# Kernel tuning notes

Measured on AMD Instinct MI355X. Metric: run time of the kernel, lower is better.

## Reference

```python
import jax, jax.numpy as jnp
import numpy as np

D_MODEL = 1024
D_FF = 4096
N_EXPERTS = 8
TOP_K = 2

def setup_inputs() -> dict:
    key = jax.random.key(0)
    ks = jax.random.split(key, 8)
    s = 1.0 / np.sqrt(D_MODEL)
    sf = 1.0 / np.sqrt(D_FF)
    return {
        "x": jax.random.normal(ks[0], (4, 1024, D_MODEL), dtype=jnp.float32),
        "W1": jax.random.uniform(ks[1], (N_EXPERTS, D_MODEL, D_FF), jnp.float32, -s, s),
        "b1": jax.random.uniform(ks[2], (N_EXPERTS, D_FF), jnp.float32, -s, s),
        "W2": jax.random.uniform(ks[3], (N_EXPERTS, D_FF, D_MODEL), jnp.float32, -sf, sf),
        "b2": jax.random.uniform(ks[4], (N_EXPERTS, D_MODEL), jnp.float32, -sf, sf),
        "Wg": jax.random.uniform(ks[5], (D_MODEL, N_EXPERTS), jnp.float32, -s, s),
        "bg": jax.random.uniform(ks[6], (N_EXPERTS,), jnp.float32, -s, s),
    }

def reference(x, W1, b1, W2, b2, Wg, bg):
    # gate: [B,S,E]
    logits = jnp.einsum('bsd,de->bse', x, Wg) + bg
    probs = jax.nn.softmax(logits, axis=-1)
    # top-k mask + renormalize (k < n_experts)
    topk_vals, topk_idx = jax.lax.top_k(probs, TOP_K)
    mask = jax.nn.one_hot(topk_idx, N_EXPERTS, dtype=probs.dtype).sum(axis=-2)
    probs = probs * mask
    denom = probs.sum(axis=-1, keepdims=True)
    denom = denom + (denom == 0).astype(probs.dtype)
    probs = probs / denom
    # dense expert compute: all experts on all tokens. h: [B,E,S,d_ff]
    h = jnp.einsum('bsd,edf->besf', x, W1) + b1[None, :, None, :]
    h = jax.nn.gelu(h, approximate=False)
    y = jnp.einsum('besf,efd->besd', h, W2) + b2[None, :, None, :]
    # weighted combine over experts: [B,S,d]
    out = jnp.einsum('bse,besd->bsd', probs, y)
    return out
```

## Files before the change

### kernel.cpp

```cpp
#include <hip/hip_runtime.h>
#include <hip/hip_bf16.h>

#define NTOK   4096
#define DMODEL 1024
#define DFF    4096
#define NEXP   8
#define TOPK   2
#define BM 128
#define BN 128
#define BK 64
#define NSLOT   (NTOK*TOPK)
#define MAXSLOT (NSLOT + NEXP*BM)
#define MAXTILE (MAXSLOT/BM)

typedef __attribute__((ext_vector_type(8))) short bf16x8;
typedef __attribute__((ext_vector_type(4))) float f32x4;

__device__ __forceinline__ unsigned short f2bf(float f){
    union { float f; unsigned int u; } v; v.f = f;
    unsigned int r = (v.u + 0x7fffu + ((v.u >> 16) & 1u)) >> 16;
    return (unsigned short)r;
}
__device__ __forceinline__ float bf2f(unsigned short h){
    union { unsigned int u; float f; } v; v.u = ((unsigned int)h) << 16;
    return v.f;
}

__device__ __forceinline__ void gload16(const unsigned short* g, unsigned short* l){
    __builtin_amdgcn_global_load_lds(
        (const __attribute__((address_space(1))) void*)g,
        (__attribute__((address_space(3))) void*)l,
        16, 0, 0);
}

__global__ __launch_bounds__(256) void k_convert(const float* __restrict__ src,
                                                 unsigned short* __restrict__ dst, int n4)
{
    int i = blockIdx.x*256 + threadIdx.x;
    if(i >= n4) return;
    float4 v = ((const float4*)src)[i];
    ushort4 o;
    o.x = f2bf(v.x); o.y = f2bf(v.y); o.z = f2bf(v.z); o.w = f2bf(v.w);
    ((ushort4*)dst)[i] = o;
}

__global__ __launch_bounds__(256) void k_transpose_convert(const float* __restrict__ src,
                                                           unsigned short* __restrict__ dst,
                                                           int R, int C)
{
    __shared__ unsigned short tile[64][72];
    src += (size_t)blockIdx.z * R * C;
    dst += (size_t)blockIdx.z * R * C;
    int r0 = blockIdx.y * 64, c0 = blockIdx.x * 64;
    int t = threadIdx.x;
    int tr = t >> 4;
    int tc = (t & 15) * 4;
    #pragma unroll
    for(int i=0;i<4;i++){
        float4 v = *(const float4*)&src[(size_t)(r0 + tr + i*16)*C + c0 + tc];
        tile[tc+0][tr + i*16] = f2bf(v.x);
        tile[tc+1][tr + i*16] = f2bf(v.y);
        tile[tc+2][tr + i*16] = f2bf(v.z);
        tile[tc+3][tr + i*16] = f2bf(v.w);
    }
    __syncthreads();
    #pragma unroll
    for(int i=0;i<4;i++){
        ushort4 o;
        o.x = tile[tr + i*16][tc+0];
        o.y = tile[tr + i*16][tc+1];
        o.z = tile[tr + i*16][tc+2];
        o.w = tile[tr + i*16][tc+3];
        *(ushort4*)&dst[(size_t)(c0 + tr + i*16)*R + r0 + tc] = o;
    }
}

__global__ __launch_bounds__(256) void k_gate(const float* __restrict__ x,
                                              const float* __restrict__ Wg,
                                              const float* __restrict__ bg,
                                              int* __restrict__ token_e,
                                              float* __restrict__ token_w,
                                              int* __restrict__ cnt)
{
    int wid = threadIdx.x >> 6, lane = threadIdx.x & 63;
    int t = blockIdx.x * 4 + wid;
    const float* xr = x + (size_t)t * DMODEL;
    float pe[NEXP];
    #pragma unroll
    for(int e=0;e<NEXP;e++) pe[e] = 0.f;
    for(int i=0;i<DMODEL/64;i++){
        int d = i*64 + lane;
        float xv = xr[d];
        const float* wr = Wg + (size_t)d * NEXP;
        #pragma unroll
        for(int e=0;e<NEXP;e++) pe[e] += xv * wr[e];
    }
    #pragma unroll
    for(int off=32; off>0; off>>=1){
        #pragma unroll
        for(int e=0;e<NEXP;e++) pe[e] += __shfl_xor(pe[e], off);
    }
    if(lane == 0){
        float lg[NEXP], mx = -1e30f;
        #pragma unroll
        for(int e=0;e<NEXP;e++){ lg[e] = pe[e] + bg[e]; mx = fmaxf(mx, lg[e]); }
        float pr[NEXP];
        #pragma unroll
        for(int e=0;e<NEXP;e++) pr[e] = expf(lg[e] - mx);
        int e0 = 0; float p0 = pr[0];
        #pragma unroll
        for(int e=1;e<NEXP;e++) if(pr[e] > p0){ p0 = pr[e]; e0 = e; }
        int e1 = -1; float p1 = -1.f;
        #pragma unroll
        for(int e=0;e<NEXP;e++) if(e != e0 && pr[e] > p1){ p1 = pr[e]; e1 = e; }
        float dn = p0 + p1;
        token_e[2*t]   = e0; token_w[2*t]   = p0/dn;
        token_e[2*t+1] = e1; token_w[2*t+1] = p1/dn;
        atomicAdd(&cnt[e0], 1); atomicAdd(&cnt[e1], 1);
    }
}

__global__ void k_prefix(const int* __restrict__ cnt, int* __restrict__ base,
                         int* __restrict__ cursor, int* __restrict__ tile_e,
                         int* __restrict__ tile_row0, int* __restrict__ tile_valid)
{
    if(threadIdx.x != 0 || blockIdx.x != 0) return;
    int off = 0, nt = 0;
    for(int e=0;e<NEXP;e++){
        base[e] = off; cursor[e] = 0;
        int c = cnt[e];
        for(int r=0;r<c;r+=BM){
            tile_e[nt] = e; tile_row0[nt] = off + r;
            tile_valid[nt] = (c - r < BM) ? (c - r) : BM;
            nt++;
        }
        off += ((c + BM - 1)/BM)*BM;
    }
    for(int i=nt;i<MAXTILE;i++){ tile_e[i]=0; tile_row0[i]=0; tile_valid[i]=0; }
}

__global__ __launch_bounds__(256) void k_scatter(const int* __restrict__ token_e,
                                                 const float* __restrict__ token_w,
                                                 const int* __restrict__ base,
                                                 int* __restrict__ cursor,
                                                 int* __restrict__ slot_token,
                                                 float* __restrict__ slot_w,
                                                 int* __restrict__ slot_of)
{
    int i = blockIdx.x*256 + threadIdx.x;
    if(i >= NSLOT) return;
    int e = token_e[i];
    int s = base[e] + atomicAdd(&cursor[e], 1);
    slot_token[s] = i >> 1;
    slot_w[s] = token_w[i];
    slot_of[i] = s;
}

template<bool GATHER, bool GELU>
__global__ __launch_bounds__(256) void k_gemm(const unsigned short* __restrict__ A,
                                              const unsigned short* __restrict__ Bw,
                                              const float* __restrict__ bias,
                                              const int* __restrict__ tile_e,
                                              const int* __restrict__ tile_row0,
                                              const int* __restrict__ tile_valid,
                                              const int* __restrict__ slot_token,
                                              const float* __restrict__ slot_w,
                                              unsigned short* __restrict__ Out,
                                              int K, int N)
{
    int tid = blockIdx.x;
    int valid = tile_valid[tid];
    if(valid == 0) return;
    int e = tile_e[tid];
    int row0 = tile_row0[tid];
    int n0 = blockIdx.y * BN;
    const unsigned short* Be = Bw + (size_t)e * N * K;

    __shared__ unsigned short As[BM*BK];
    __shared__ unsigned short Bs[BN*BK];

    int t = threadIdx.x;
    int lane = t & 63;
    int wid = t >> 6;
    int wr = wid >> 1, wc = wid & 1;

    int srow = t >> 3;
    int csw  = (t & 7) ^ (srow & 7);
    const unsigned short* arow[4];
    const unsigned short* brow[4];
    #pragma unroll
    for(int i=0;i<4;i++){
        int r = i*32 + srow;
        size_t aoff;
        if(GATHER) aoff = (size_t)slot_token[row0 + r] * (size_t)K;
        else       aoff = (size_t)(row0 + r) * (size_t)K;
        arow[i] = A  + aoff + csw*8;
        brow[i] = Be + (size_t)(n0 + r)*K + csw*8;
    }
    unsigned short* alds = As + (size_t)t * 8;
    unsigned short* blds = Bs + (size_t)t * 8;

    f32x4 acc[4][4];
    #pragma unroll
    for(int m=0;m<4;m++)
        #pragma unroll
        for(int n=0;n<4;n++)
            acc[m][n] = (f32x4){0.f,0.f,0.f,0.f};

    int rl = lane & 15;
    int g  = lane >> 4;
    int rx = rl & 7;

    for(int k0=0;k0<K;k0+=BK){
        __syncthreads();
        #pragma unroll
        for(int i=0;i<4;i++){
            gload16(arow[i] + k0, alds + i*2048);
            gload16(brow[i] + k0, blds + i*2048);
        }
        __syncthreads();

        #pragma unroll
        for(int kb=0;kb<2;kb++){
            int sw = ((kb*4 + g) ^ rx) * 8;
            bf16x8 af[4], bfv[4];
            #pragma unroll
            for(int m=0;m<4;m++) af[m]  = *(const bf16x8*)&As[(wr*64 + m*16 + rl)*BK + sw];
            #pragma unroll
            for(int n=0;n<4;n++) bfv[n] = *(const bf16x8*)&Bs[(wc*64 + n*16 + rl)*BK + sw];
            #pragma unroll
            for(int m=0;m<4;m++)
                #pragma unroll
                for(int n=0;n<4;n++)
                    acc[m][n] = __builtin_amdgcn_mfma_f32_16x16x32_bf16(af[m], bfv[n], acc[m][n], 0, 0, 0);
        }
    }

    const float* be = bias + (size_t)e * N;
    #pragma unroll
    for(int m=0;m<4;m++){
        int rb = wr*64 + m*16 + ((lane>>4)<<2);
        #pragma unroll
        for(int j=0;j<4;j++){
            int r = rb + j;
            if(r >= valid) continue;
            size_t grow = (size_t)(row0 + r);
            float wsc = GELU ? 0.f : slot_w[grow];
            #pragma unroll
            for(int n=0;n<4;n++){
                int col = n0 + wc*64 + n*16 + (lane & 15);
                float v = acc[m][n][j] + be[col];
                if(GELU) v = 0.5f * v * (1.f + erff(v * 0.70710678118654752f));
                else     v *= wsc;
                Out[grow * (size_t)N + col] = f2bf(v);
            }
        }
    }
}

__global__ __launch_bounds__(256) void k_combine(const int* __restrict__ slot_of,
                                                 const unsigned short* __restrict__ Y,
                                                 float* __restrict__ out)
{
    int i = blockIdx.x*256 + threadIdx.x;
    int t  = i >> 8;
    int cg = i & 255;
    int s0 = slot_of[2*t], s1 = slot_of[2*t+1];
    uint2 a = *((const uint2*)(Y + (size_t)s0*DMODEL) + cg);
    uint2 b = *((const uint2*)(Y + (size_t)s1*DMODEL) + cg);
    float4 o;
    o.x = bf2f((unsigned short)(a.x & 0xffffu)) + bf2f((unsigned short)(b.x & 0xffffu));
    o.y = bf2f((unsigned short)(a.x >> 16))     + bf2f((unsigned short)(b.x >> 16));
    o.z = bf2f((unsigned short)(a.y & 0xffffu)) + bf2f((unsigned short)(b.y & 0xffffu));
    o.w = bf2f((unsigned short)(a.y >> 16))     + bf2f((unsigned short)(b.y >> 16));
    *((float4*)(out + (size_t)t*DMODEL) + cg) = o;
}

extern "C" void kernel_launch(void* const* d_in, const int* in_sizes, int n_in,
                              void* d_out, int out_size, void* d_ws, size_t ws_size,
                              hipStream_t stream)
{
    const float* x  = (const float*)d_in[0];
    const float* W1 = (const float*)d_in[1];
    const float* b1 = (const float*)d_in[2];
    const float* W2 = (const float*)d_in[3];
    const float* b2 = (const float*)d_in[4];
    const float* Wg = (const float*)d_in[5];
    const float* bg = (const float*)d_in[6];
    float* out = (float*)d_out;

    char* p = (char*)d_ws;
    auto alloc = [&](size_t bytes)->char*{
        char* r = p; p += (bytes + 255) & ~(size_t)255; return r;
    };
    unsigned short* W1t = (unsigned short*)alloc((size_t)NEXP*DFF*DMODEL*2);
    unsigned short* W2t = (unsigned short*)alloc((size_t)NEXP*DMODEL*DFF*2);
    unsigned short* Xb  = (unsigned short*)alloc((size_t)NTOK*DMODEL*2);
    unsigned short* H   = (unsigned short*)alloc((size_t)MAXSLOT*DFF*2);
    unsigned short* Y   = (unsigned short*)alloc((size_t)MAXSLOT*DMODEL*2);
    int*   slot_token = (int*)alloc(MAXSLOT*4);
    float* slot_w     = (float*)alloc(MAXSLOT*4);
    int*   slot_of    = (int*)alloc(NSLOT*4);
    int*   token_e    = (int*)alloc(NSLOT*4);
    float* token_w    = (float*)alloc(NSLOT*4);
    int*   cnt    = (int*)alloc(32);
    int*   base   = (int*)alloc(32);
    int*   cursor = (int*)alloc(32);
    int*   tile_e     = (int*)alloc(MAXTILE*4);
    int*   tile_row0  = (int*)alloc(MAXTILE*4);
    int*   tile_valid = (int*)alloc(MAXTILE*4);
    (void)ws_size; (void)in_sizes; (void)n_in; (void)out_size;

    hipMemsetAsync(cnt, 0, 32, stream);
    hipMemsetAsync(slot_token, 0, MAXSLOT*4, stream);
    k_convert<<<(NTOK*DMODEL/4 + 255)/256, 256, 0, stream>>>(x, Xb, NTOK*DMODEL/4);
    k_transpose_convert<<<dim3(DFF/64, DMODEL/64, NEXP), 256, 0, stream>>>(W1, W1t, DMODEL, DFF);
    k_transpose_convert<<<dim3(DMODEL/64, DFF/64, NEXP), 256, 0, stream>>>(W2, W2t, DFF, DMODEL);
    k_gate<<<NTOK/4, 256, 0, stream>>>(x, Wg, bg, token_e, token_w, cnt);
    k_prefix<<<1, 64, 0, stream>>>(cnt, base, cursor, tile_e, tile_row0, tile_valid);
    k_scatter<<<NSLOT/256, 256, 0, stream>>>(token_e, token_w, base, cursor,
                                             slot_token, slot_w, slot_of);
    k_gemm<true, true ><<<dim3(MAXTILE, DFF/BN),    256, 0, stream>>>(
        Xb, W1t, b1, tile_e, tile_row0, tile_valid, slot_token, slot_w, H, DMODEL, DFF);
    k_gemm<false,false><<<dim3(MAXTILE, DMODEL/BN), 256, 0, stream>>>(
        H,  W2t, b2, tile_e, tile_row0, tile_valid, slot_token, slot_w, Y, DFF, DMODEL);
    k_combine<<<NTOK*DMODEL/4/256, 256, 0, stream>>>(slot_of, Y, out);
}
```

Baseline: 496.1 us.

## Rewrite grouped GEMM as 256x256 tile, 8-wave double-buffered pipelined MFMA kernel

Grows the expert GEMM tile to 256x256 with 512 threads and eight waves. Global-to-LDS loads are double-buffered and interleaved with MFMA phases, using explicit waitcnt, barriers and setprio so loads overlap compute. The x bf16 conversion moves into the gate kernel, prefix and scatter merge into one single-block kernel, and Y reuses the W1t buffer. Larger tiles raise data reuse but pad each expert group to 256 rows, which wastes more work, and the single-block scatter serialises that step.

```diff
diff --git a/kernel.cpp b/kernel.cpp
--- a/kernel.cpp
+++ b/kernel.cpp
@@ -6,9 +6,8 @@
 #define DFF    4096
 #define NEXP   8
 #define TOPK   2
-#define BM 128
-#define BN 128
-#define BK 64
+#define BM 256
+#define BN 256
 #define NSLOT   (NTOK*TOPK)
 #define MAXSLOT (NSLOT + NEXP*BM)
 #define MAXTILE (MAXSLOT/BM)
@@ -33,15 +32,15 @@
         16, 0, 0);
 }
 
-__global__ __launch_bounds__(256) void k_convert(const float* __restrict__ src,
-                                                 unsigned short* __restrict__ dst, int n4)
-{
-    int i = blockIdx.x*256 + threadIdx.x;
-    if(i >= n4) return;
-    float4 v = ((const float4*)src)[i];
-    ushort4 o;
-    o.x = f2bf(v.x); o.y = f2bf(v.y); o.z = f2bf(v.z); o.w = f2bf(v.w);
-    ((ushort4*)dst)[i] = o;
+#define WAITLGKM() asm volatile("s_waitcnt lgkmcnt(0)" ::: "memory")
+#define WAITVM4()  asm volatile("s_waitcnt vmcnt(4)" ::: "memory")
+#define WAITVM0()  asm volatile("s_waitcnt vmcnt(0)" ::: "memory")
+#define MFMA16(a,b,c) __builtin_amdgcn_mfma_f32_16x16x32_bf16(a,b,c,0,0,0)
+
+__device__ __forceinline__ bf16x8 ldswz(const unsigned short* lds, int base, int r, int kcol){
+    int idx = base + r*64 + kcol;
+    idx ^= ((r>>2)&1) << 4;
+    return *(const bf16x8*)&lds[idx];
 }
 
 __global__ __launch_bounds__(256) void k_transpose_convert(const float* __restrict__ src,
@@ -78,11 +77,22 @@
 __global__ __launch_bounds__(256) void k_gate(const float* __restrict__ x,
                                               const float* __restrict__ Wg,
                                               const float* __restrict__ bg,
+                                              unsigned short* __restrict__ Xb,
                                               int* __restrict__ token_e,
                                               float* __restrict__ token_w,
                                               int* __restrict__ cnt)
 {
-    int wid = threadIdx.x >> 6, lane = threadIdx.x & 63;
+    int tid = threadIdx.x;
+    const float4* xs = (const float4*)x + (size_t)blockIdx.x * 1024;
+    ushort4* xd = (ushort4*)Xb + (size_t)blockIdx.x * 1024;
+    #pragma unroll
+    for(int rep=0;rep<4;rep++){
+        float4 v = xs[rep*256 + tid];
+        ushort4 o; o.x=f2bf(v.x); o.y=f2bf(v.y); o.z=f2bf(v.z); o.w=f2bf(v.w);
+        xd[rep*256 + tid] = o;
+    }
+
+    int wid = tid >> 6, lane = tid & 63;
     int t = blockIdx.x * 4 + wid;
     const float* xr = x + (size_t)t * DMODEL;
     float pe[NEXP];
@@ -120,136 +130,204 @@
     }
 }
 
-__global__ void k_prefix(const int* __restrict__ cnt, int* __restrict__ base,
-                         int* __restrict__ cursor, int* __restrict__ tile_e,
-                         int* __restrict__ tile_row0, int* __restrict__ tile_valid)
-{
-    if(threadIdx.x != 0 || blockIdx.x != 0) return;
-    int off = 0, nt = 0;
-    for(int e=0;e<NEXP;e++){
-        base[e] = off; cursor[e] = 0;
-        int c = cnt[e];
-        for(int r=0;r<c;r+=BM){
-            tile_e[nt] = e; tile_row0[nt] = off + r;
-            tile_valid[nt] = (c - r < BM) ? (c - r) : BM;
-            nt++;
-        }
-        off += ((c + BM - 1)/BM)*BM;
-    }
-    for(int i=nt;i<MAXTILE;i++){ tile_e[i]=0; tile_row0[i]=0; tile_valid[i]=0; }
-}
-
-__global__ __launch_bounds__(256) void k_scatter(const int* __restrict__ token_e,
-                                                 const float* __restrict__ token_w,
-                                                 const int* __restrict__ base,
-                                                 int* __restrict__ cursor,
-                                                 int* __restrict__ slot_token,
-                                                 float* __restrict__ slot_w,
-                                                 int* __restrict__ slot_of)
-{
-    int i = blockIdx.x*256 + threadIdx.x;
-    if(i >= NSLOT) return;
-    int e = token_e[i];
-    int s = base[e] + atomicAdd(&cursor[e], 1);
-    slot_token[s] = i >> 1;
-    slot_w[s] = token_w[i];
-    slot_of[i] = s;
+__global__ __launch_bounds__(256) void k_prefix_scatter(const int* __restrict__ cnt,
+                                                        const int* __restrict__ token_e,
+                                                        const float* __restrict__ token_w,
+                                                        int* __restrict__ tile_e,
+                                                        int* __restrict__ tile_row0,
+                                                        int* __restrict__ tile_valid,
+                                                        int* __restrict__ slot_token,
+                                                        float* __restrict__ slot_w,
+                                                        int* __restrict__ slot_of)
+{
+    __shared__ int sb[NEXP], scur[NEXP];
+    int tid = threadIdx.x;
+    if(tid == 0){
+        int off = 0, nt = 0;
+        for(int e=0;e<NEXP;e++){
+            sb[e] = off; scur[e] = 0;
+            int c = cnt[e];
+            for(int r=0;r<c;r+=BM){
+                tile_e[nt] = e; tile_row0[nt] = off + r;
+                tile_valid[nt] = (c - r < BM) ? (c - r) : BM;
+                nt++;
+            }
+            off += ((c + BM - 1)/BM)*BM;
+        }
+        for(int i=nt;i<MAXTILE;i++){ tile_e[i]=0; tile_row0[i]=0; tile_valid[i]=0; }
+    }
+    for(int s=tid; s<MAXSLOT; s+=256) slot_token[s] = 0;
+    __syncthreads();
+    for(int i=tid; i<NSLOT; i+=256){
+        int e = token_e[i];
+        int s = sb[e] + atomicAdd(&scur[e], 1);
+        slot_token[s] = i >> 1;
+        slot_w[s] = token_w[i];
+        slot_of[i] = s;
+    }
 }
 
 template<bool GATHER, bool GELU>
-__global__ __launch_bounds__(256) void k_gemm(const unsigned short* __restrict__ A,
-                                              const unsigned short* __restrict__ Bw,
-                                              const float* __restrict__ bias,
-                                              const int* __restrict__ tile_e,
-                                              const int* __restrict__ tile_row0,
-                                              const int* __restrict__ tile_valid,
-                                              const int* __restrict__ slot_token,
-                                              const float* __restrict__ slot_w,
-                                              unsigned short* __restrict__ Out,
-                                              int K, int N)
-{
-    int tid = blockIdx.x;
-    int valid = tile_valid[tid];
+__global__ __launch_bounds__(512, 2) void k_gemm(const unsigned short* __restrict__ A,
+                                                 const unsigned short* __restrict__ Bw,
+                                                 const float* __restrict__ bias,
+                                                 const int* __restrict__ tile_e,
+                                                 const int* __restrict__ tile_row0,
+                                                 const int* __restrict__ tile_valid,
+                                                 const int* __restrict__ slot_token,
+                                                 const float* __restrict__ slot_w,
+                                                 unsigned short* __restrict__ Out,
+                                                 int K, int N)
+{
+    int tb = blockIdx.x;
+    int valid = tile_valid[tb];
     if(valid == 0) return;
-    int e = tile_e[tid];
-    int row0 = tile_row0[tid];
+    int e = tile_e[tb], row0 = tile_row0[tb];
     int n0 = blockIdx.y * BN;
     const unsigned short* Be = Bw + (size_t)e * N * K;
 
-    __shared__ unsigned short As[BM*BK];
-    __shared__ unsigned short Bs[BN*BK];
-
-    int t = threadIdx.x;
-    int lane = t & 63;
-    int wid = t >> 6;
-    int wr = wid >> 1, wc = wid & 1;
-
-    int srow = t >> 3;
-    int csw  = (t & 7) ^ (srow & 7);
-    const unsigned short* arow[4];
-    const unsigned short* brow[4];
-    #pragma unroll
-    for(int i=0;i<4;i++){
-        int r = i*32 + srow;
-        size_t aoff;
-        if(GATHER) aoff = (size_t)slot_token[row0 + r] * (size_t)K;
-        else       aoff = (size_t)(row0 + r) * (size_t)K;
-        arow[i] = A  + aoff + csw*8;
-        brow[i] = Be + (size_t)(n0 + r)*K + csw*8;
-    }
-    unsigned short* alds = As + (size_t)t * 8;
-    unsigned short* blds = Bs + (size_t)t * 8;
-
-    f32x4 acc[4][4];
-    #pragma unroll
-    for(int m=0;m<4;m++)
-        #pragma unroll
-        for(int n=0;n<4;n++)
-            acc[m][n] = (f32x4){0.f,0.f,0.f,0.f};
-
-    int rl = lane & 15;
-    int g  = lane >> 4;
-    int rx = rl & 7;
-
-    for(int k0=0;k0<K;k0+=BK){
-        __syncthreads();
-        #pragma unroll
-        for(int i=0;i<4;i++){
-            gload16(arow[i] + k0, alds + i*2048);
-            gload16(brow[i] + k0, blds + i*2048);
-        }
-        __syncthreads();
-
-        #pragma unroll
-        for(int kb=0;kb<2;kb++){
-            int sw = ((kb*4 + g) ^ rx) * 8;
-            bf16x8 af[4], bfv[4];
+    __shared__ unsigned short lds[65536];
+
+    int tid = threadIdx.x;
+    int lane = tid & 63, wid = tid >> 6;
+    int wm = wid >> 2, wn = wid & 3;
+    int rl = lane & 15, g = lane >> 4;
+
+    int r8  = tid >> 3;
+    int ccs = (tid & 7) ^ (((tid >> 5) & 1) << 1);
+    const unsigned short* asrc[2][2];
+    const unsigned short* bsrc[2][2];
+    #pragma unroll
+    for(int h=0;h<2;h++){
+        #pragma unroll
+        for(int l=0;l<2;l++){
+            int r = h*128 + l*64 + r8;
+            size_t ar = GATHER ? (size_t)slot_token[row0 + r] * (size_t)K
+                               : (size_t)(row0 + r) * (size_t)K;
+            asrc[h][l] = A  + ar + ccs*8;
+            bsrc[h][l] = Be + (size_t)(n0 + r)*K + ccs*8;
+        }
+    }
+    int ldst = tid * 8;
+
+#define SA(kt,h,l) gload16(asrc[h][l] + (kt)*64, &lds[(((kt)&1)<<15) + ((h)<<13) + ((l)<<12) + ldst])
+#define SB(kt,h,l) gload16(bsrc[h][l] + (kt)*64, &lds[(((kt)&1)<<15) + 16384 + ((h)<<13) + ((l)<<12) + ldst])
+
+    SA(0,0,0); SA(0,0,1); SA(0,1,0); SA(0,1,1);
+    SB(0,0,0); SB(0,0,1); SB(0,1,0); SB(0,1,1);
+    SB(1,0,0); SB(1,0,1); SB(1,1,0); SB(1,1,1);
+
+    f32x4 acc[8][4];
+    #pragma unroll
+    for(int i=0;i<8;i++)
+        #pragma unroll
+        for(int j=0;j<4;j++) acc[i][j] = (f32x4){0.f,0.f,0.f,0.f};
+
+    WAITVM4();
+    __builtin_amdgcn_s_barrier();
+
+    int NK = K >> 6;
+    bf16x8 af[4][2], bfv[4][2];
+
+    for(int k=0;k<NK;k++){
+        int bufo = (k & 1) << 15;
+        bool stA = (k+1 < NK);
+        bool stB = (k+2 < NK);
+
+        #pragma unroll
+        for(int m=0;m<4;m++){
+            af[m][0] = ldswz(lds, bufo, wm*128 + m*16 + rl, g*8);
+            af[m][1] = ldswz(lds, bufo, wm*128 + m*16 + rl, 32 + g*8);
+        }
+        #pragma unroll
+        for(int n=0;n<2;n++){
+            bfv[n][0] = ldswz(lds, bufo + 16384, wn*64 + n*16 + rl, g*8);
+            bfv[n][1] = ldswz(lds, bufo + 16384, wn*64 + n*16 + rl, 32 + g*8);
+        }
+        if(stA){ SA(k+1,0,0); SA(k+1,0,1); }
+        __builtin_amdgcn_s_barrier();
+        WAITLGKM();
+        __builtin_amdgcn_s_setprio(1);
+        #pragma unroll
+        for(int m=0;m<4;m++)
             #pragma unroll
-            for(int m=0;m<4;m++) af[m]  = *(const bf16x8*)&As[(wr*64 + m*16 + rl)*BK + sw];
+            for(int n=0;n<2;n++){
+                acc[m][n] = MFMA16(af[m][0], bfv[n][0], acc[m][n]);
+                acc[m][n] = MFMA16(af[m][1], bfv[n][1], acc[m][n]);
+            }
+        __builtin_amdgcn_s_setprio(0);
+        __builtin_amdgcn_s_barrier();
+
+        #pragma unroll
+        for(int n=2;n<4;n++){
+            bfv[n][0] = ldswz(lds, bufo + 16384, wn*64 + n*16 + rl, g*8);
+            bfv[n][1] = ldswz(lds, bufo + 16384, wn*64 + n*16 + rl, 32 + g*8);
+        }
+        if(stA){ SA(k+1,1,0); SA(k+1,1,1); }
+        __builtin_amdgcn_s_barrier();
+        WAITLGKM();
+        __builtin_amdgcn_s_setprio(1);
+        #pragma unroll
+        for(int m=0;m<4;m++)
             #pragma unroll
-            for(int n=0;n<4;n++) bfv[n] = *(const bf16x8*)&Bs[(wc*64 + n*16 + rl)*BK + sw];
+            for(int n=2;n<4;n++){
+                acc[m][n] = MFMA16(af[m][0], bfv[n][0], acc[m][n]);
+                acc[m][n] = MFMA16(af[m][1], bfv[n][1], acc[m][n]);
+            }
+        __builtin_amdgcn_s_setprio(0);
+        __builtin_amdgcn_s_barrier();
+
+        #pragma unroll
+        for(int m=0;m<4;m++){
+            af[m][0] = ldswz(lds, bufo, wm*128 + 64 + m*16 + rl, g*8);
+            af[m][1] = ldswz(lds, bufo, wm*128 + 64 + m*16 + rl, 32 + g*8);
+        }
+        if(stB){ SB(k+2,0,0); SB(k+2,0,1); }
+        __builtin_amdgcn_s_barrier();
+        WAITLGKM();
+        __builtin_amdgcn_s_setprio(1);
+        #pragma unroll
+        for(int m=0;m<4;m++)
             #pragma unroll
-            for(int m=0;m<4;m++)
-                #pragma unroll
-                for(int n=0;n<4;n++)
-                    acc[m][n] = __builtin_amdgcn_mfma_f32_16x16x32_bf16(af[m], bfv[n], acc[m][n], 0, 0, 0);
-        }
-    }
+            for(int n=0;n<2;n++){
+                acc[4+m][n] = MFMA16(af[m][0], bfv[n][0], acc[4+m][n]);
+                acc[4+m][n] = MFMA16(af[m][1], bfv[n][1], acc[4+m][n]);
+            }
+        __builtin_amdgcn_s_setprio(0);
+        __builtin_amdgcn_s_barrier();
+
+        if(stB){ SB(k+2,1,0); SB(k+2,1,1); }
+        __builtin_amdgcn_s_barrier();
+        __builtin_amdgcn_s_setprio(1);
+        #pragma unroll
+        for(int m=0;m<4;m++)
+            #pragma unroll
+            for(int n=2;n<4;n++){
+                acc[4+m][n] = MFMA16(af[m][0], bfv[n][0], acc[4+m][n]);
+                acc[4+m][n] = MFMA16(af[m][1], bfv[n][1], acc[4+m][n]);
+            }
+        __builtin_amdgcn_s_setprio(0);
+        if(stB)      { WAITVM4(); }
+        else if(stA) { WAITVM0(); }
+        __builtin_amdgcn_s_barrier();
+    }
+#undef SA
+#undef SB
 
     const float* be = bias + (size_t)e * N;
     #pragma unroll
-    for(int m=0;m<4;m++){
-        int rb = wr*64 + m*16 + ((lane>>4)<<2);
+    for(int mi=0;mi<8;mi++){
+        int rbase = wm*128 + mi*16 + g*4;
         #pragma unroll
         for(int j=0;j<4;j++){
-            int r = rb + j;
+            int r = rbase + j;
             if(r >= valid) continue;
             size_t grow = (size_t)(row0 + r);
             float wsc = GELU ? 0.f : slot_w[grow];
             #pragma unroll
             for(int n=0;n<4;n++){
-                int col = n0 + wc*64 + n*16 + (lane & 15);
-                float v = acc[m][n][j] + be[col];
+                int col = n0 + wn*64 + n*16 + rl;
+                float v = acc[mi][n][j] + be[col];
                 if(GELU) v = 0.5f * v * (1.f + erff(v * 0.70710678118654752f));
                 else     v *= wsc;
                 Out[grow * (size_t)N + col] = f2bf(v);
@@ -297,32 +375,28 @@
     unsigned short* W2t = (unsigned short*)alloc((size_t)NEXP*DMODEL*DFF*2);
     unsigned short* Xb  = (unsigned short*)alloc((size_t)NTOK*DMODEL*2);
     unsigned short* H   = (unsigned short*)alloc((size_t)MAXSLOT*DFF*2);
-    unsigned short* Y   = (unsigned short*)alloc((size_t)MAXSLOT*DMODEL*2);
+    unsigned short* Y   = W1t;
     int*   slot_token = (int*)alloc(MAXSLOT*4);
     float* slot_w     = (float*)alloc(MAXSLOT*4);
     int*   slot_of    = (int*)alloc(NSLOT*4);
     int*   token_e    = (int*)alloc(NSLOT*4);
     float* token_w    = (float*)alloc(NSLOT*4);
-    int*   cnt    = (int*)alloc(32);
-    int*   base   = (int*)alloc(32);
-    int*   cursor = (int*)alloc(32);
+    int*   cnt        = (int*)alloc(32);
     int*   tile_e     = (int*)alloc(MAXTILE*4);
     int*   tile_row0  = (int*)alloc(MAXTILE*4);
     int*   tile_valid = (int*)alloc(MAXTILE*4);
     (void)ws_size; (void)in_sizes; (void)n_in; (void)out_size;
 
     hipMemsetAsync(cnt, 0, 32, stream);
-    hipMemsetAsync(slot_token, 0, MAXSLOT*4, stream);
-    k_convert<<<(NTOK*DMODEL/4 + 255)/256, 256, 0, stream>>>(x, Xb, NTOK*DMODEL/4);
+    k_gate<<<NTOK/4, 256, 0, stream>>>(x, Wg, bg, Xb, token_e, token_w, cnt);
     k_transpose_convert<<<dim3(DFF/64, DMODEL/64, NEXP), 256, 0, stream>>>(W1, W1t, DMODEL, DFF);
     k_transpose_convert<<<dim3(DMODEL/64, DFF/64, NEXP), 256, 0, stream>>>(W2, W2t, DFF, DMODEL);
-    k_gate<<<NTOK/4, 256, 0, stream>>>(x, Wg, bg, token_e, token_w, cnt);
-    k_prefix<<<1, 64, 0, stream>>>(cnt, base, cursor, tile_e, tile_row0, tile_valid);
-    k_scatter<<<NSLOT/256, 256, 0, stream>>>(token_e, token_w, base, cursor,
-                                             slot_token, slot_w, slot_of);
-    k_gemm<true, true ><<<dim3(MAXTILE, DFF/BN),    256, 0, stream>>>(
+    k_prefix_scatter<<<1, 256, 0, stream>>>(cnt, token_e, token_w,
+                                            tile_e, tile_row0, tile_valid,
+                                            slot_token, slot_w, slot_of);
+    k_gemm<true, true ><<<dim3(MAXTILE, DFF/BN),    512, 0, stream>>>(
         Xb, W1t, b1, tile_e, tile_row0, tile_valid, slot_token, slot_w, H, DMODEL, DFF);
-    k_gemm<false,false><<<dim3(MAXTILE, DMODEL/BN), 256, 0, stream>>>(
+    k_gemm<false,false><<<dim3(MAXTILE, DMODEL/BN), 512, 0, stream>>>(
         H,  W2t, b2, tile_e, tile_row0, tile_valid, slot_token, slot_w, Y, DFF, DMODEL);
     k_combine<<<NTOK*DMODEL/4/256, 256, 0, stream>>>(slot_of, Y, out);
 }
```

After: 535.8 us. 1.08x slower.

## Fuse combine into second GEMM via atomics and merge small setup kernels

Applied to the files above, without the earlier changes.

The second expert GEMM now scales its results by the routing weight and atomically adds them straight into the fp32 output, which is zeroed beforehand. This removes the Y buffer and the separate combine kernel. The x-to-bf16 conversion moves into the gate kernel, prefix and scatter become one single-block kernel with shared-memory cursors, and the transpose kernel now writes 16-byte vectors. The cost is fp32 atomic contention on the output, a memset of the whole output, and a serial single-block scatter over 8192 slots.

```diff
diff --git a/kernel.cpp b/kernel.cpp
--- a/kernel.cpp
+++ b/kernel.cpp
@@ -14,16 +14,13 @@
 #define MAXTILE (MAXSLOT/BM)
 
 typedef __attribute__((ext_vector_type(8))) short bf16x8;
+typedef __attribute__((ext_vector_type(8))) unsigned short u16x8;
 typedef __attribute__((ext_vector_type(4))) float f32x4;
 
 __device__ __forceinline__ unsigned short f2bf(float f){
     union { float f; unsigned int u; } v; v.f = f;
     unsigned int r = (v.u + 0x7fffu + ((v.u >> 16) & 1u)) >> 16;
     return (unsigned short)r;
-}
-__device__ __forceinline__ float bf2f(unsigned short h){
-    union { unsigned int u; float f; } v; v.u = ((unsigned int)h) << 16;
-    return v.f;
 }
 
 __device__ __forceinline__ void gload16(const unsigned short* g, unsigned short* l){
@@ -31,17 +28,6 @@
         (const __attribute__((address_space(1))) void*)g,
         (__attribute__((address_space(3))) void*)l,
         16, 0, 0);
-}
-
-__global__ __launch_bounds__(256) void k_convert(const float* __restrict__ src,
-                                                 unsigned short* __restrict__ dst, int n4)
-{
-    int i = blockIdx.x*256 + threadIdx.x;
-    if(i >= n4) return;
-    float4 v = ((const float4*)src)[i];
-    ushort4 o;
-    o.x = f2bf(v.x); o.y = f2bf(v.y); o.z = f2bf(v.z); o.w = f2bf(v.w);
-    ((ushort4*)dst)[i] = o;
 }
 
 __global__ __launch_bounds__(256) void k_transpose_convert(const float* __restrict__ src,
@@ -64,25 +50,34 @@
         tile[tc+3][tr + i*16] = f2bf(v.w);
     }
     __syncthreads();
-    #pragma unroll
-    for(int i=0;i<4;i++){
-        ushort4 o;
-        o.x = tile[tr + i*16][tc+0];
-        o.y = tile[tr + i*16][tc+1];
-        o.z = tile[tr + i*16][tc+2];
-        o.w = tile[tr + i*16][tc+3];
-        *(ushort4*)&dst[(size_t)(c0 + tr + i*16)*R + r0 + tc] = o;
+    int rr  = t >> 3;
+    int cc8 = (t & 7) * 8;
+    #pragma unroll
+    for(int i=0;i<2;i++){
+        u16x8 o = *(const u16x8*)&tile[rr + i*32][cc8];
+        *(u16x8*)&dst[(size_t)(c0 + rr + i*32)*R + r0 + cc8] = o;
     }
 }
 
 __global__ __launch_bounds__(256) void k_gate(const float* __restrict__ x,
                                               const float* __restrict__ Wg,
                                               const float* __restrict__ bg,
+                                              unsigned short* __restrict__ Xb,
                                               int* __restrict__ token_e,
                                               float* __restrict__ token_w,
                                               int* __restrict__ cnt)
 {
-    int wid = threadIdx.x >> 6, lane = threadIdx.x & 63;
+    int tid = threadIdx.x;
+    const float4* xs = (const float4*)x + (size_t)blockIdx.x * 1024;
+    ushort4* xd = (ushort4*)Xb + (size_t)blockIdx.x * 1024;
+    #pragma unroll
+    for(int rep=0;rep<4;rep++){
+        float4 v = xs[rep*256 + tid];
+        ushort4 o; o.x=f2bf(v.x); o.y=f2bf(v.y); o.z=f2bf(v.z); o.w=f2bf(v.w);
+        xd[rep*256 + tid] = o;
+    }
+
+    int wid = tid >> 6, lane = tid & 63;
     int t = blockIdx.x * 4 + wid;
     const float* xr = x + (size_t)t * DMODEL;
     float pe[NEXP];
@@ -120,40 +115,39 @@
     }
 }
 
-__global__ void k_prefix(const int* __restrict__ cnt, int* __restrict__ base,
-                         int* __restrict__ cursor, int* __restrict__ tile_e,
-                         int* __restrict__ tile_row0, int* __restrict__ tile_valid)
-{
-    if(threadIdx.x != 0 || blockIdx.x != 0) return;
-    int off = 0, nt = 0;
-    for(int e=0;e<NEXP;e++){
-        base[e] = off; cursor[e] = 0;
-        int c = cnt[e];
-        for(int r=0;r<c;r+=BM){
-            tile_e[nt] = e; tile_row0[nt] = off + r;
-            tile_valid[nt] = (c - r < BM) ? (c - r) : BM;
-            nt++;
+__global__ __launch_bounds__(256) void k_prefix_scatter(const int* __restrict__ cnt,
+                                                        const int* __restrict__ token_e,
+                                                        const float* __restrict__ token_w,
+                                                        int* __restrict__ tile_e,
+                                                        int* __restrict__ tile_row0,
+                                                        int* __restrict__ tile_valid,
+                                                        int* __restrict__ slot_token,
+                                                        float* __restrict__ slot_w)
+{
+    __shared__ int sb[NEXP], scur[NEXP];
+    int tid = threadIdx.x;
+    if(tid == 0){
+        int off = 0, nt = 0;
+        for(int e=0;e<NEXP;e++){
+            sb[e] = off; scur[e] = 0;
+            int c = cnt[e];
+            for(int r=0;r<c;r+=BM){
+                tile_e[nt] = e; tile_row0[nt] = off + r;
+                tile_valid[nt] = (c - r < BM) ? (c - r) : BM;
+                nt++;
+            }
+            off += ((c + BM - 1)/BM)*BM;
         }
-        off += ((c + BM - 1)/BM)*BM;
-    }
-    for(int i=nt;i<MAXTILE;i++){ tile_e[i]=0; tile_row0[i]=0; tile_valid[i]=0; }
-}
-
-__global__ __launch_bounds__(256) void k_scatter(const int* __restrict__ token_e,
-                                                 const float* __restrict__ token_w,
-                                                 const int* __restrict__ base,
-                                                 int* __restrict__ cursor,
-                                                 int* __restrict__ slot_token,
-                                                 float* __restrict__ slot_w,
-                                                 int* __restrict__ slot_of)
-{
-    int i = blockIdx.x*256 + threadIdx.x;
-    if(i >= NSLOT) return;
-    int e = token_e[i];
-    int s = base[e] + atomicAdd(&cursor[e], 1);
-    slot_token[s] = i >> 1;
-    slot_w[s] = token_w[i];
-    slot_of[i] = s;
+        for(int i=nt;i<MAXTILE;i++){ tile_e[i]=0; tile_row0[i]=0; tile_valid[i]=0; }
+    }
+    for(int s=tid; s<MAXSLOT; s+=256) slot_token[s] = 0;
+    __syncthreads();
+    for(int i=tid; i<NSLOT; i+=256){
+        int e = token_e[i];
+        int s = sb[e] + atomicAdd(&scur[e], 1);
+        slot_token[s] = i >> 1;
+        slot_w[s] = token_w[i];
+    }
 }
 
 template<bool GATHER, bool GELU>
@@ -165,7 +159,8 @@
                                               const int* __restrict__ tile_valid,
                                               const int* __restrict__ slot_token,
                                               const float* __restrict__ slot_w,
-                                              unsigned short* __restrict__ Out,
+                                              unsigned short* __restrict__ OutH,
+                                              float* __restrict__ outF,
                                               int K, int N)
 {
     int tid = blockIdx.x;
@@ -245,35 +240,26 @@
             int r = rb + j;
             if(r >= valid) continue;
             size_t grow = (size_t)(row0 + r);
-            float wsc = GELU ? 0.f : slot_w[grow];
-            #pragma unroll
-            for(int n=0;n<4;n++){
-                int col = n0 + wc*64 + n*16 + (lane & 15);
-                float v = acc[m][n][j] + be[col];
-                if(GELU) v = 0.5f * v * (1.f + erff(v * 0.70710678118654752f));
-                else     v *= wsc;
-                Out[grow * (size_t)N + col] = f2bf(v);
+            if(GELU){
+                #pragma unroll
+                for(int n=0;n<4;n++){
+                    int col = n0 + wc*64 + n*16 + rl;
+                    float v = acc[m][n][j] + be[col];
+                    v = 0.5f * v * (1.f + erff(v * 0.70710678118654752f));
+                    OutH[grow * (size_t)N + col] = f2bf(v);
+                }
+            } else {
+                float wsc = slot_w[grow];
+                float* orow = outF + (size_t)slot_token[grow] * DMODEL;
+                #pragma unroll
+                for(int n=0;n<4;n++){
+                    int col = n0 + wc*64 + n*16 + rl;
+                    float v = (acc[m][n][j] + be[col]) * wsc;
+                    atomicAdd(&orow[col], v);
+                }
             }
         }
     }
-}
-
-__global__ __launch_bounds__(256) void k_combine(const int* __restrict__ slot_of,
-                                                 const unsigned short* __restrict__ Y,
-                                                 float* __restrict__ out)
-{
-    int i = blockIdx.x*256 + threadIdx.x;
-    int t  = i >> 8;
-    int cg = i & 255;
-    int s0 = slot_of[2*t], s1 = slot_of[2*t+1];
-    uint2 a = *((const uint2*)(Y + (size_t)s0*DMODEL) + cg);
-    uint2 b = *((const uint2*)(Y + (size_t)s1*DMODEL) + cg);
-    float4 o;
-    o.x = bf2f((unsigned short)(a.x & 0xffffu)) + bf2f((unsigned short)(b.x & 0xffffu));
-    o.y = bf2f((unsigned short)(a.x >> 16))     + bf2f((unsigned short)(b.x >> 16));
-    o.z = bf2f((unsigned short)(a.y & 0xffffu)) + bf2f((unsigned short)(b.y & 0xffffu));
-    o.w = bf2f((unsigned short)(a.y >> 16))     + bf2f((unsigned short)(b.y >> 16));
-    *((float4*)(out + (size_t)t*DMODEL) + cg) = o;
 }
 
 extern "C" void kernel_launch(void* const* d_in, const int* in_sizes, int n_in,
@@ -297,32 +283,26 @@
     unsigned short* W2t = (unsigned short*)alloc((size_t)NEXP*DMODEL*DFF*2);
     unsigned short* Xb  = (unsigned short*)alloc((size_t)NTOK*DMODEL*2);
     unsigned short* H   = (unsigned short*)alloc((size_t)MAXSLOT*DFF*2);
-    unsigned short* Y   = (unsigned short*)alloc((size_t)MAXSLOT*DMODEL*2);
     int*   slot_token = (int*)alloc(MAXSLOT*4);
     float* slot_w     = (float*)alloc(MAXSLOT*4);
-    int*   slot_of    = (int*)alloc(NSLOT*4);
     int*   token_e    = (int*)alloc(NSLOT*4);
     float* token_w    = (float*)alloc(NSLOT*4);
-    int*   cnt    = (int*)alloc(32);
-    int*   base   = (int*)alloc(32);
-    int*   cursor = (int*)alloc(32);
+    int*   cnt        = (int*)alloc(32);
     int*   tile_e     = (int*)alloc(MAXTILE*4);
     int*   tile_row0  = (int*)alloc(MAXTILE*4);
     int*   tile_valid = (int*)alloc(MAXTILE*4);
     (void)ws_size; (void)in_sizes; (void)n_in; (void)out_size;
 
     hipMemsetAsync(cnt, 0, 32, stream);
-    hipMemsetAsync(slot_token, 0, MAXSLOT*4, stream);
-    k_convert<<<(NTOK*DMODEL/4 + 255)/256, 256, 0, stream>>>(x, Xb, NTOK*DMODEL/4);
+    hipMemsetAsync(out, 0, (size_t)NTOK*DMODEL*4, stream);
+    k_gate<<<NTOK/4, 256, 0, stream>>>(x, Wg, bg, Xb, token_e, token_w, cnt);
     k_transpose_convert<<<dim3(DFF/64, DMODEL/64, NEXP), 256, 0, stream>>>(W1, W1t, DMODEL, DFF);
     k_transpose_convert<<<dim3(DMODEL/64, DFF/64, NEXP), 256, 0, stream>>>(W2, W2t, DFF, DMODEL);
-    k_gate<<<NTOK/4, 256, 0, stream>>>(x, Wg, bg, token_e, token_w, cnt);
-    k_prefix<<<1, 64, 0, stream>>>(cnt, base, cursor, tile_e, tile_row0, tile_valid);
-    k_scatter<<<NSLOT/256, 256, 0, stream>>>(token_e, token_w, base, cursor,
-                                             slot_token, slot_w, slot_of);
+    k_prefix_scatter<<<1, 256, 0, stream>>>(cnt, token_e, token_w,
+                                            tile_e, tile_row0, tile_valid,
+                                            slot_token, slot_w);
     k_gemm<true, true ><<<dim3(MAXTILE, DFF/BN),    256, 0, stream>>>(
-        Xb, W1t, b1, tile_e, tile_row0, tile_valid, slot_token, slot_w, H, DMODEL, DFF);
+        Xb, W1t, b1, tile_e, tile_row0, tile_valid, slot_token, slot_w, H, nullptr, DMODEL, DFF);
     k_gemm<false,false><<<dim3(MAXTILE, DMODEL/BN), 256, 0, stream>>>(
-        H,  W2t, b2, tile_e, tile_row0, tile_valid, slot_token, slot_w, Y, DFF, DMODEL);
-    k_combine<<<NTOK*DMODEL/4/256, 256, 0, stream>>>(slot_of, Y, out);
-}
+        H,  W2t, b2, tile_e, tile_row0, tile_valid, slot_token, slot_w, nullptr, out, DFF, DMODEL);
+}
```

After: 502.6 us. Within noise of the previous version (+1.3%).
